# Optimization experiments

Measured on AMD Instinct MI355X. Metric: run time of the kernel, lower is better.

Reference implementation:

```python
import jax, jax.numpy as jnp
import numpy as np

NUM_TOKENS = 32000
N_EMBD = 2048
N_HEAD = 16
HEAD_SIZE = N_EMBD // N_HEAD
MAX_LEN = 2048
SEQ = 2048


def _make_pe(max_len, d_model):
    position = np.arange(max_len, dtype=np.float32)[:, None]
    emb_idx = np.arange(0, d_model, 2, dtype=np.float32)
    div_term = 1.0 / np.power(10000.0, emb_idx / d_model)
    pe = np.zeros((max_len, d_model), dtype=np.float32)
    pe[:, 0::2] = np.sin(position * div_term)
    pe[:, 1::2] = np.cos(position * div_term)
    return jnp.asarray(pe)


def setup_inputs() -> dict:
    key = jax.random.key(0)
    ks = jax.random.split(key, 8)
    s = 1.0 / np.sqrt(N_EMBD)
    return {
        "token_ids": jax.random.randint(ks[0], (SEQ,), 0, NUM_TOKENS, dtype=jnp.int32),
        "we": jax.random.normal(ks[1], (NUM_TOKENS, N_EMBD), dtype=jnp.float32),
        "pe": _make_pe(MAX_LEN, N_EMBD),
        "Wq": jax.random.normal(ks[2], (N_HEAD, N_EMBD, HEAD_SIZE), dtype=jnp.float32) * s,
        "Wk": jax.random.normal(ks[3], (N_HEAD, N_EMBD, HEAD_SIZE), dtype=jnp.float32) * s,
        "Wv": jax.random.normal(ks[4], (N_HEAD, N_EMBD, HEAD_SIZE), dtype=jnp.float32) * s,
        "proj_w": jax.random.normal(ks[5], (N_EMBD, N_EMBD), dtype=jnp.float32) * s,
        "proj_b": jnp.zeros((N_EMBD,), dtype=jnp.float32),
        "fc_w": jax.random.normal(ks[6], (N_EMBD, NUM_TOKENS), dtype=jnp.float32) * s,
        "fc_b": jnp.zeros((NUM_TOKENS,), dtype=jnp.float32),
    }


def reference(token_ids, we, pe, Wq, Wk, Wv, proj_w, proj_b, fc_w, fc_b):
    T = token_ids.shape[0]
    x = we[token_ids] + pe[:T]                      # [T, D]
    # per-head QKV, stacked over heads: [H, T, hs]
    q = jnp.einsum('td,hdk->htk', x, Wq)
    k = jnp.einsum('td,hdk->htk', x, Wk)
    v = jnp.einsum('td,hdk->htk', x, Wv)
    scale = 1.0 / jnp.sqrt(jnp.asarray(HEAD_SIZE, dtype=x.dtype))
    sims = jnp.einsum('htk,hsk->hts', q, k) * scale  # [H, T, T]
    causal = jnp.tril(jnp.ones((T, T), dtype=bool))  # mask==0 where NOT lower-tri
    sims = jnp.where(causal[None], sims, jnp.asarray(-1e9, dtype=x.dtype))
    attn = jax.nn.softmax(sims, axis=-1)
    heads = jnp.einsum('hts,hsk->htk', attn, v)      # [H, T, hs]
    cat = jnp.transpose(heads, (1, 0, 2)).reshape(T, N_HEAD * HEAD_SIZE)
    sa = cat @ proj_w + proj_b                       # dropout = identity (eval)
    resid = x + sa
    return resid @ fc_w + fc_b                       # [T, num_tokens]
```

## Files before the change

kernel.cpp:

```cpp
#include <hip/hip_runtime.h>

#define T_SEQ 2048
#define D_EMB 2048
#define NHEAD 16
#define HS    128
#define NVOC  32000

typedef __attribute__((ext_vector_type(8))) short bf16x8;
typedef __attribute__((ext_vector_type(4))) float f32x4;
typedef unsigned short bfu;

__device__ __forceinline__ f32x4 mfma16(bf16x8 a, bf16x8 b, f32x4 c) {
    return __builtin_amdgcn_mfma_f32_16x16x32_bf16(a, b, c, 0, 0, 0);
}

__device__ __forceinline__ bfu f2bu(float f) {
    unsigned int u = __float_as_uint(f);
    unsigned int r = (u + 0x7fffu + ((u >> 16) & 1u)) >> 16;
    return (bfu)r;
}
__device__ __forceinline__ float b2f(bfu r) {
    return __uint_as_float((unsigned int)r << 16);
}

__device__ __forceinline__ void async_copy16(void* lds, const void* g) {
    __builtin_amdgcn_global_load_lds(
        (const __attribute__((address_space(1))) unsigned int*)g,
        (__attribute__((address_space(3))) unsigned int*)lds, 16, 0, 0);
}

#define SB0 __builtin_amdgcn_sched_barrier(0)
#define BARRIER __builtin_amdgcn_s_barrier()
#define WAIT_VM8   asm volatile("s_waitcnt vmcnt(8)" ::: "memory")
#define WAIT_VM6   asm volatile("s_waitcnt vmcnt(6)" ::: "memory")
#define WAIT_VM4   asm volatile("s_waitcnt vmcnt(4)" ::: "memory")
#define WAIT_VM2   asm volatile("s_waitcnt vmcnt(2)" ::: "memory")
#define WAIT_VM0   asm volatile("s_waitcnt vmcnt(0)" ::: "memory")

__device__ __forceinline__ void job_t64(const float* __restrict__ in,
                                        bfu* __restrict__ out, int R, int C,
                                        float scale, int tx, int ty, char* lds) {
    float (*tile)[65] = (float(*)[65])lds;
    const int r0 = ty * 64, c0 = tx * 64;
    const int t = threadIdx.x;
#pragma unroll
    for (int it = 0; it < 4; ++it) {
        int fi = it * 256 + t;
        int row = fi >> 4, c4 = (fi & 15) * 4;
        float4 v = *(const float4*)(in + (size_t)(r0 + row) * C + c0 + c4);
        tile[row][c4]     = v.x; tile[row][c4 + 1] = v.y;
        tile[row][c4 + 2] = v.z; tile[row][c4 + 3] = v.w;
    }
    __syncthreads();
#pragma unroll
    for (int it = 0; it < 4; ++it) {
        int ci = it * 256 + t;
        int oc = ci >> 4, r4 = (ci & 15) * 4;
        ushort4 u;
        u.x = f2bu(tile[r4 + 0][oc] * scale);
        u.y = f2bu(tile[r4 + 1][oc] * scale);
        u.z = f2bu(tile[r4 + 2][oc] * scale);
        u.w = f2bu(tile[r4 + 3][oc] * scale);
        *(ushort4*)(out + (size_t)(c0 + oc) * R + r0 + r4) = u;
    }
}

__global__ __launch_bounds__(256)
void k_prep(const int* __restrict__ ids, const float* __restrict__ we,
            const float* __restrict__ pe, bfu* __restrict__ xb,
            const float* __restrict__ Wq, const float* __restrict__ Wk,
            const float* __restrict__ Wv, const float* __restrict__ projw,
            bfu* __restrict__ WqT, bfu* __restrict__ WkT, bfu* __restrict__ WvT,
            bfu* __restrict__ projT, float qscale) {
    __shared__ __align__(16) char lds[64 * 65 * 4];
    int b = blockIdx.x;
    if (b < 1024) {
        job_t64(projw, projT, D_EMB, D_EMB, 1.0f, b & 31, b >> 5, lds);
    } else if (b < 4096) {
        int bb = b - 1024;
        int which = bb >> 10;
        bb &= 1023;
        int z = bb >> 6, rem = bb & 63;
        size_t zo = (size_t)z * D_EMB * HS;
        const float* in = (which == 0) ? Wq : (which == 1) ? Wk : Wv;
        bfu* out = (which == 0) ? WqT : (which == 1) ? WkT : WvT;
        job_t64(in + zo, out + zo, D_EMB, HS, (which == 0) ? qscale : 1.0f,
                rem & 1, rem >> 1, lds);
    } else {
        int tt = b - 4096;
        const int row = ids[tt];
        const float4* wr = (const float4*)(we + (size_t)row * D_EMB);
        const float4* pr = (const float4*)(pe + (size_t)tt * D_EMB);
        bfu* xbr = xb + (size_t)tt * D_EMB;
        int i = threadIdx.x;
#pragma unroll
        for (int r = 0; r < 2; ++r, i += 256) {
            float4 a = wr[i], p = pr[i];
            ushort4 u;
            u.x = f2bu(a.x + p.x); u.y = f2bu(a.y + p.y);
            u.z = f2bu(a.z + p.z); u.w = f2bu(a.w + p.w);
            *(ushort4*)(xbr + i * 4) = u;
        }
    }
}

__global__ void k_transpose_bf(const bfu* __restrict__ in, bfu* __restrict__ out,
                               int stride, int Tout) {
    __shared__ bfu tile[64][72];
    const int r0 = blockIdx.x * 64;
    const int c0 = blockIdx.y * 64;
    const int t = threadIdx.x;
#pragma unroll
    for (int it = 0; it < 2; ++it) {
        int idx = it * 256 + t;
        int row = idx >> 3, c8 = (idx & 7) * 8;
        *(bf16x8*)&tile[row][c8] = *(const bf16x8*)(in + (size_t)(r0 + row) * stride + c0 + c8);
    }
    __syncthreads();
#pragma unroll
    for (int it = 0; it < 2; ++it) {
        int idx = it * 256 + t;
        int oc = idx >> 3, r8 = (idx & 7) * 8;
        bf16x8 v;
#pragma unroll
        for (int j = 0; j < 8; ++j) v[j] = (short)tile[r8 + j][oc];
        *(bf16x8*)(out + (size_t)(c0 + oc) * Tout + r0 + r8) = v;
    }
}

template <int EPI>
__global__ __launch_bounds__(256, 2)
void k_gemm_nt(const bfu* __restrict__ A, const bfu* __restrict__ Bt,
               bfu* __restrict__ Cv, const float* __restrict__ bias,
               const bfu* __restrict__ resb, int M, int N, int K) {
    __shared__ __align__(16) char smem[2 * 128 * 64 * 2];
    const int tid = threadIdx.x;
    const int w = tid >> 6, lane = tid & 63;
    const int wr = w >> 1, wc = w & 1;
    const int lr = lane & 15, lk = lane >> 4;
    const int sw = ((lk ^ (lr & 7)) << 4);
    const int mb = M >> 7;
    const int m0 = (blockIdx.x % mb) << 7;
    const int n0 = (blockIdx.x / mb) << 7;
    char* As = smem;
    char* Bs = smem + 16384;
    f32x4 acc[4][4];
#pragma unroll
    for (int i = 0; i < 4; ++i)
#pragma unroll
        for (int j = 0; j < 4; ++j) acc[i][j] = (f32x4){0.f, 0.f, 0.f, 0.f};

    const bfu* Ag = A + (size_t)m0 * K;
    const bfu* Bg = Bt + (size_t)n0 * K;

    for (int kk = 0; kk < K; kk += 64) {
        __syncthreads();
#pragma unroll
        for (int r = 0; r < 4; ++r) {
            int i = r * 256 + tid;
            int row = i >> 3, slot = (i & 7) ^ (row & 7);
            async_copy16(As + (r * 256 + w * 64) * 16,
                         Ag + (size_t)row * K + kk + slot * 8);
        }
#pragma unroll
        for (int r = 0; r < 4; ++r) {
            int i = r * 256 + tid;
            int row = i >> 3, slot = (i & 7) ^ (row & 7);
            async_copy16(Bs + (r * 256 + w * 64) * 16,
                         Bg + (size_t)row * K + kk + slot * 8);
        }
        __syncthreads();
#pragma unroll
        for (int kc = 0; kc < 2; ++kc) {
            const int so = kc ? (sw ^ 64) : sw;
            bf16x8 a[4], b[4];
#pragma unroll
            for (int mf = 0; mf < 4; ++mf)
                a[mf] = *(const bf16x8*)(As + (wr * 64 + mf * 16 + lr) * 128 + so);
#pragma unroll
            for (int nf = 0; nf < 4; ++nf)
                b[nf] = *(const bf16x8*)(Bs + (wc * 64 + nf * 16 + lr) * 128 + so);
#pragma unroll
            for (int mf = 0; mf < 4; ++mf)
#pragma unroll
                for (int nf = 0; nf < 4; ++nf)
                    acc[mf][nf] = mfma16(a[mf], b[nf], acc[mf][nf]);
        }
    }
#pragma unroll
    for (int nf = 0; nf < 4; ++nf) {
        int col = n0 + wc * 64 + nf * 16 + lr;
        float bv = (EPI >= 1) ? bias[col] : 0.0f;
#pragma unroll
        for (int mf = 0; mf < 4; ++mf) {
            int row0 = m0 + wr * 64 + mf * 16 + lk * 4;
            f32x4 v = acc[mf][nf];
#pragma unroll
            for (int j = 0; j < 4; ++j) {
                size_t idx = (size_t)(row0 + j) * N + col;
                float val = v[j] + bv;
                if (EPI == 1) val += b2f(resb[idx]);
                Cv[idx] = f2bu(val);
            }
        }
    }
}

__device__ __forceinline__ void stage_chunk(char* sm, const bfu* A_, const bfu* B_,
                                            int K, int tt, int kind, int w,
                                            int laneRow, int laneCol) {
    char* base = sm + (size_t)(tt & 1) * 65536 + ((kind >= 2) ? 32768 : 0);
    const bfu* G = (kind >= 2) ? B_ : A_;
#pragma unroll
    for (int r = 0; r < 2; ++r) {
        int p = w * 2 + r;
        int row0 = (kind < 2) ? ((kind & 1) * 64 + (p & 7) * 8 + (p >> 3) * 128)
                              : ((kind & 1) * 32 + (p & 3) * 8 + (p >> 2) * 64);
        const char* g = (const char*)G + ((size_t)(row0 + laneRow) * K + tt * 64) * 2 + laneCol;
        async_copy16(base + row0 * 128, g);
    }
}

template <int Q>
__device__ __forceinline__ void read_A(bf16x8 (&aA)[2][4][2], const char* bufA,
                                       int wm, int lr, int sw0) {
    const char* p = bufA + ((wm * 128 + Q * 64 + lr) * 128);
#pragma unroll
    for (int mf = 0; mf < 4; ++mf) {
        aA[Q][mf][0] = *(const bf16x8*)(p + mf * 2048 + sw0);
        aA[Q][mf][1] = *(const bf16x8*)(p + mf * 2048 + (sw0 ^ 64));
    }
}

template <int Q>
__device__ __forceinline__ void read_B(bf16x8 (&bB)[2][2], const char* bufB,
                                       int wn, int lr, int sw0) {
    const char* p = bufB + ((wn * 64 + Q * 32 + lr) * 128);
#pragma unroll
    for (int nf = 0; nf < 2; ++nf) {
        bB[nf][0] = *(const bf16x8*)(p + nf * 2048 + sw0);
        bB[nf][1] = *(const bf16x8*)(p + nf * 2048 + (sw0 ^ 64));
    }
}

template <int QM, int QN>
__device__ __forceinline__ void mfma_quad(f32x4 (&acc)[8][4], bf16x8 (&aA)[2][4][2],
                                          bf16x8 (&bB)[2][2]) {
    __builtin_amdgcn_s_setprio(1);
#pragma unroll
    for (int kc = 0; kc < 2; ++kc)
#pragma unroll
        for (int mf = 0; mf < 4; ++mf)
#pragma unroll
            for (int nf = 0; nf < 2; ++nf)
                acc[QM * 4 + mf][QN * 2 + nf] =
                    mfma16(aA[QM][mf][kc], bB[nf][kc], acc[QM * 4 + mf][QN * 2 + nf]);
    __builtin_amdgcn_s_setprio(0);
}

__device__ __forceinline__ void job_fcw512(const float* __restrict__ in,
                                           bfu* __restrict__ out, int tx, int ty,
                                           char* lds) {
    const int r0 = ty * 256, c0 = tx * 64;
    const int t = threadIdx.x;
#pragma unroll
    for (int it = 0; it < 8; ++it) {
        int fi = it * 512 + t;
        int row = fi >> 4, c4 = (fi & 15) * 4;
        float4 v = *(const float4*)(in + (size_t)(r0 + row) * NVOC + c0 + c4);
        ushort4 u;
        u.x = f2bu(v.x); u.y = f2bu(v.y); u.z = f2bu(v.z); u.w = f2bu(v.w);
        *(ushort4*)(lds + row * 128 + ((c4 * 2) ^ (((row >> 3) & 7) << 4))) = u;
    }
    __syncthreads();
#pragma unroll
    for (int it = 0; it < 4; ++it) {
        int idx = it * 512 + t;
        int oc = idx >> 5, r8 = (idx & 31) * 8;
        bf16x8 v;
#pragma unroll
        for (int j = 0; j < 8; ++j) {
            int row = r8 + j;
            v[j] = (short)*(const bfu*)(lds + row * 128 +
                                        ((oc * 2) ^ (((row >> 3) & 7) << 4)));
        }
        *(bf16x8*)(out + (size_t)(c0 + oc) * D_EMB + r0 + r8) = v;
    }
}

template <int EPI, bool FUSE_FCW>
__global__ __launch_bounds__(512, 2)
void k_gemm256(const bfu* __restrict__ A, const bfu* __restrict__ Bt,
               void* __restrict__ Cv, const float* __restrict__ bias,
               int M, int N, int K,
               const float* __restrict__ fcw, bfu* __restrict__ fcwT,
               int gemm_nwgs) {
    __shared__ __align__(16) char smem[2 * 65536];
    if (FUSE_FCW && (int)blockIdx.x >= gemm_nwgs) {
        int fb = blockIdx.x - gemm_nwgs;
        job_fcw512(fcw, fcwT, fb % 500, fb / 500, smem);
        return;
    }
    const int tid = threadIdx.x;
    const int w = tid >> 6, lane = tid & 63;
    const int wm = w >> 2, wn = w & 3;
    const int lr = lane & 15, lk = lane >> 4;
    const int sw0 = ((lk ^ (lr & 7)) << 4);
    const int laneRow = lane >> 3;
    const int laneCol = ((lane & 7) ^ (lane >> 3)) << 4;

    const int mb = M >> 8;
    const int nwgs = mb * (N >> 8);
    int bid = blockIdx.x;
    int swz = ((nwgs & 7) == 0) ? ((bid & 7) * (nwgs >> 3) + (bid >> 3)) : bid;
    const int m0 = (swz % mb) << 8;
    const int n0 = (swz / mb) << 8;

    const bfu* Ag = A + (size_t)m0 * K;
    const bfu* Bg = Bt + (size_t)n0 * K;

    f32x4 acc[8][4];
#pragma unroll
    for (int i = 0; i < 8; ++i)
#pragma unroll
        for (int j = 0; j < 4; ++j) acc[i][j] = (f32x4){0.f, 0.f, 0.f, 0.f};
    bf16x8 aA[2][4][2], bB[2][2];

    const int nkt = K >> 6;

    stage_chunk(smem, Ag, Bg, K, 0, 0, w, laneRow, laneCol);
    stage_chunk(smem, Ag, Bg, K, 0, 2, w, laneRow, laneCol);
    stage_chunk(smem, Ag, Bg, K, 0, 1, w, laneRow, laneCol);
    stage_chunk(smem, Ag, Bg, K, 0, 3, w, laneRow, laneCol);
    stage_chunk(smem, Ag, Bg, K, 1, 2, w, laneRow, laneCol);
    stage_chunk(smem, Ag, Bg, K, 1, 0, w, laneRow, laneCol);
    WAIT_VM8; SB0; BARRIER;

    for (int t = 0; t < nkt - 2; ++t) {
        const char* bufA = smem + (size_t)(t & 1) * 65536;
        const char* bufB = bufA + 32768;
        read_A<0>(aA, bufA, wm, lr, sw0);
        read_B<0>(bB, bufB, wn, lr, sw0);
        stage_chunk(smem, Ag, Bg, K, t + 1, 1, w, laneRow, laneCol);
        mfma_quad<0, 0>(acc, aA, bB);
        WAIT_VM8; BARRIER;

        read_A<1>(aA, bufA, wm, lr, sw0);
        stage_chunk(smem, Ag, Bg, K, t + 1, 3, w, laneRow, laneCol);
        mfma_quad<1, 0>(acc, aA, bB);
        WAIT_VM8; BARRIER;

        read_B<1>(bB, bufB, wn, lr, sw0);
        stage_chunk(smem, Ag, Bg, K, t + 2, 2, w, laneRow, laneCol);
        mfma_quad<0, 1>(acc, aA, bB);
        WAIT_VM8; BARRIER;

        stage_chunk(smem, Ag, Bg, K, t + 2, 0, w, laneRow, laneCol);
        mfma_quad<1, 1>(acc, aA, bB);
        WAIT_VM8; BARRIER;
    }

    {
        const int t = nkt - 2;
        const char* bufA = smem + (size_t)(t & 1) * 65536;
        const char* bufB = bufA + 32768;
        read_A<0>(aA, bufA, wm, lr, sw0);
        read_B<0>(bB, bufB, wn, lr, sw0);
        stage_chunk(smem, Ag, Bg, K, t + 1, 1, w, laneRow, laneCol);
        mfma_quad<0, 0>(acc, aA, bB);
        WAIT_VM8; BARRIER;

        read_A<1>(aA, bufA, wm, lr, sw0);
        stage_chunk(smem, Ag, Bg, K, t + 1, 3, w, laneRow, laneCol);
        mfma_quad<1, 0>(acc, aA, bB);
        WAIT_VM8; BARRIER;

        read_B<1>(bB, bufB, wn, lr, sw0);
        mfma_quad<0, 1>(acc, aA, bB);
        WAIT_VM6; BARRIER;

        mfma_quad<1, 1>(acc, aA, bB);
        WAIT_VM4; BARRIER;
    }
    {
        const int t = nkt - 1;
        const char* bufA = smem + (size_t)(t & 1) * 65536;
        const char* bufB = bufA + 32768;
        read_A<0>(aA, bufA, wm, lr, sw0);
        read_B<0>(bB, bufB, wn, lr, sw0);
        mfma_quad<0, 0>(acc, aA, bB);
        WAIT_VM2; BARRIER;

        read_A<1>(aA, bufA, wm, lr, sw0);
        mfma_quad<1, 0>(acc, aA, bB);
        WAIT_VM0; BARRIER;

        read_B<1>(bB, bufB, wn, lr, sw0);
        mfma_quad<0, 1>(acc, aA, bB);
        mfma_quad<1, 1>(acc, aA, bB);
    }

#pragma unroll
    for (int nfg = 0; nfg < 4; ++nfg) {
        int col = n0 + wn * 64 + nfg * 16 + lr;
        float bv = (EPI == 2) ? bias[col] : 0.0f;
#pragma unroll
        for (int mfg = 0; mfg < 8; ++mfg) {
            int row0 = m0 + wm * 128 + mfg * 16 + lk * 4;
            f32x4 v = acc[mfg][nfg];
#pragma unroll
            for (int j = 0; j < 4; ++j) {
                size_t idx = (size_t)(row0 + j) * N + col;
                if (EPI == 2) ((float*)Cv)[idx] = v[j] + bv;
                else          ((bfu*)Cv)[idx] = f2bu(v[j]);
            }
        }
    }
}

__global__ __launch_bounds__(256, 2)
void k_attn(const bfu* __restrict__ q, const bfu* __restrict__ k,
            const bfu* __restrict__ vT, bfu* __restrict__ o, int qks) {
    __shared__ __align__(16) char kvlds[2][32768];
    __shared__ __align__(16) bfu plds[4][16][72];
    const int w = threadIdx.x >> 6, lane = threadIdx.x & 63;
    const int lr = lane & 15, lk = lane >> 4;
    const int h = blockIdx.y;
    const int bxr = (gridDim.x - 1) - blockIdx.x;
    const int qrow = bxr * 64 + w * 16;
    const int sw = ((lk ^ (lr & 7)) << 4);

    const int krow = lane >> 4, kslot = lane & 15;
    const int vrow = lane >> 3, vslot = lane & 7;

    bf16x8 aq[4];
#pragma unroll
    for (int kc = 0; kc < 4; ++kc)
        aq[kc] = *(const bf16x8*)(q + (size_t)(qrow + lr) * qks + h * HS + kc * 32 + lk * 8);

    f32x4 O[8];
#pragma unroll
    for (int hf = 0; hf < 8; ++hf) O[hf] = (f32x4){0.f, 0.f, 0.f, 0.f};
    float m_[4], l_[4];
#pragma unroll
    for (int j = 0; j < 4; ++j) { m_[j] = -__builtin_inff(); l_[j] = 0.f; }

    const int nst = bxr + 1;

#define STAGE_KV(st)                                                            \
    {                                                                           \
        char* bK = kvlds[(st) & 1];                                             \
        char* bV = bK + 16384;                                                  \
        const int s0_ = (st) * 64;                                              \
        _Pragma("unroll")                                                       \
        for (int j = 0; j < 4; ++j) {                                           \
            int ir = w * 4 + j;                                                 \
            int krw = ir * 4 + krow;                                            \
            int kss = (kslot & 8) | ((kslot & 7) ^ (krw & 7));                  \
            async_copy16(bK + ir * 1024,                                        \
                         k + (size_t)(s0_ + krw) * qks + h * HS + kss * 8);     \
            int vrw = ir * 8 + vrow;                                            \
            int vss = vslot ^ (vrw & 7);                                        \
            async_copy16(bV + ir * 1024,                                        \
                         vT + (size_t)(h * HS + vrw) * T_SEQ + s0_ + vss * 8);  \
        }                                                                       \
    }

    STAGE_KV(0);
    WAIT_VM0; BARRIER;

    for (int st = 0; st < nst; ++st) {
        const char* bK = kvlds[st & 1];
        const char* bV = bK + 16384;
        const int s0 = st * 64;
        if (st + 1 < nst) STAGE_KV(st + 1);

        f32x4 S[4];
#pragma unroll
        for (int nf = 0; nf < 4; ++nf) S[nf] = (f32x4){0.f, 0.f, 0.f, 0.f};
#pragma unroll
        for (int nf = 0; nf < 4; ++nf) {
            const char* kp = bK + (nf * 16 + lr) * 256;
#pragma unroll
            for (int kc = 0; kc < 4; ++kc) {
                bf16x8 bk = *(const bf16x8*)(kp + ((kc & 2) << 6) + (sw ^ ((kc & 1) << 6)));
                S[nf] = mfma16(aq[kc], bk, S[nf]);
            }
        }
        if (s0 + 63 > qrow) {
#pragma unroll
            for (int nf = 0; nf < 4; ++nf) {
                int scol = s0 + nf * 16 + lr;
#pragma unroll
                for (int j = 0; j < 4; ++j)
                    if (scol > qrow + lk * 4 + j) S[nf][j] = -1e30f;
            }
        }
        float tm[4];
#pragma unroll
        for (int j = 0; j < 4; ++j)
            tm[j] = fmaxf(fmaxf(S[0][j], S[1][j]), fmaxf(S[2][j], S[3][j]));
#pragma unroll
        for (int d = 1; d < 16; d <<= 1)
#pragma unroll
            for (int j = 0; j < 4; ++j) tm[j] = fmaxf(tm[j], __shfl_xor(tm[j], d));
        float mn[4], ts[4];
#pragma unroll
        for (int j = 0; j < 4; ++j) mn[j] = fmaxf(m_[j], tm[j]);
#pragma unroll
        for (int nf = 0; nf < 4; ++nf)
#pragma unroll
            for (int j = 0; j < 4; ++j) S[nf][j] = __expf(S[nf][j] - mn[j]);
#pragma unroll
        for (int j = 0; j < 4; ++j) ts[j] = S[0][j] + S[1][j] + S[2][j] + S[3][j];
#pragma unroll
        for (int d = 1; d < 16; d <<= 1)
#pragma unroll
            for (int j = 0; j < 4; ++j) ts[j] += __shfl_xor(ts[j], d);
#pragma unroll
        for (int nf = 0; nf < 4; ++nf)
#pragma unroll
            for (int j = 0; j < 4; ++j)
                plds[w][lk * 4 + j][nf * 16 + lr] = f2bu(S[nf][j]);
#pragma unroll
        for (int j = 0; j < 4; ++j) {
            float f = __expf(m_[j] - mn[j]);
            l_[j] = l_[j] * f + ts[j];
            m_[j] = mn[j];
#pragma unroll
            for (int hf = 0; hf < 8; ++hf) O[hf][j] *= f;
        }
        bf16x8 pa[2];
#pragma unroll
        for (int kc2 = 0; kc2 < 2; ++kc2)
            pa[kc2] = *(const bf16x8*)(&plds[w][lr][kc2 * 32 + lk * 8]);
#pragma unroll
        for (int hf = 0; hf < 8; ++hf) {
            const char* vp = bV + (hf * 16 + lr) * 128;
#pragma unroll
            for (int kc2 = 0; kc2 < 2; ++kc2) {
                bf16x8 bv = *(const bf16x8*)(vp + (sw ^ (kc2 << 6)));
                O[hf] = mfma16(pa[kc2], bv, O[hf]);
            }
        }
        WAIT_VM0; BARRIER;
    }
#undef STAGE_KV

#pragma unroll
    for (int j = 0; j < 4; ++j) {
        float inv = 1.0f / l_[j];
        size_t rbase = (size_t)(qrow + lk * 4 + j) * D_EMB + h * HS;
#pragma unroll
        for (int hf = 0; hf < 8; ++hf)
            o[rbase + hf * 16 + lr] = f2bu(O[hf][j] * inv);
    }
}

extern "C" void kernel_launch(void* const* d_in, const int* in_sizes, int n_in,
                              void* d_out, int out_size, void* d_ws, size_t ws_size,
                              hipStream_t stream) {
    const int*   ids   = (const int*)d_in[0];
    const float* we    = (const float*)d_in[1];
    const float* pe    = (const float*)d_in[2];
    const float* Wq    = (const float*)d_in[3];
    const float* Wk    = (const float*)d_in[4];
    const float* Wv    = (const float*)d_in[5];
    const float* projw = (const float*)d_in[6];
    const float* projb = (const float*)d_in[7];
    const float* fcw   = (const float*)d_in[8];
    const float* fcb   = (const float*)d_in[9];
    float* out = (float*)d_out;
    (void)in_sizes; (void)n_in; (void)out_size; (void)ws_size;

    char* ws = (char*)d_ws;
    size_t off = 0;
    bfu*   fcwT  = (bfu*)(ws + off);  off += (size_t)NVOC * D_EMB * 2;
    bfu*   xb    = (bfu*)(ws + off);  off += (size_t)T_SEQ * D_EMB * 2;
    bfu*   qkvb  = (bfu*)(ws + off);  off += (size_t)T_SEQ * 3 * D_EMB * 2;
    bfu*   vTb   = (bfu*)(ws + off);  off += (size_t)D_EMB * T_SEQ * 2;
    bfu*   WqT   = (bfu*)(ws + off);  off += (size_t)D_EMB * D_EMB * 2;
    bfu*   WkT   = (bfu*)(ws + off);  off += (size_t)D_EMB * D_EMB * 2;
    bfu*   WvT   = (bfu*)(ws + off);  off += (size_t)D_EMB * D_EMB * 2;
    bfu*   projT = (bfu*)(ws + off);  off += (size_t)D_EMB * D_EMB * 2;
    bfu*   attnb = WqT;
    bfu*   resb  = WvT;

    const float qscale = 0.08838834764831845f;

    k_prep<<<6144, 256, 0, stream>>>(ids, we, pe, xb, Wq, Wk, Wv, projw,
                                     WqT, WkT, WvT, projT, qscale);

    k_gemm256<0, true><<<192 + 4000, 512, 0, stream>>>(
        xb, WqT, qkvb, nullptr, T_SEQ, 3 * D_EMB, D_EMB, fcw, fcwT, 192);

    k_transpose_bf<<<dim3(T_SEQ / 64, D_EMB / 64), 256, 0, stream>>>(
        qkvb + 2 * D_EMB, vTb, 3 * D_EMB, T_SEQ);

    k_attn<<<dim3(T_SEQ / 64, NHEAD), 256, 0, stream>>>(qkvb, qkvb + D_EMB, vTb, attnb, 3 * D_EMB);

    k_gemm_nt<1><<<(T_SEQ / 128) * (D_EMB / 128), 256, 0, stream>>>(
        attnb, projT, resb, projb, xb, T_SEQ, D_EMB, D_EMB);

    k_gemm256<2, false><<<(T_SEQ / 256) * (NVOC / 256), 512, 0, stream>>>(
        resb, fcwT, out, fcb, T_SEQ, NVOC, D_EMB, nullptr, nullptr, 0);
}
```

Measured before the change: 568.0 us.

## Prefetch next-tile LDS fragments into double-buffered registers during MFMA quads

Gives the B fragments a second register buffer (one per half-tile) so each quad reads the next A/B half from LDS before issuing the current MFMAs. The first-quad fragments of the next k-tile are loaded early, during the last quad of the current tile, and the wait counts and barriers are reshuffled to match, with one barrier dropping its vmcnt wait. The aim is to hide LDS read latency behind MFMA work. It costs more VGPRs and adds a risk of subtle read/write hazards on the shared buffers if the barrier placement is wrong.

```diff
diff --git a/kernel.cpp b/kernel.cpp
--- a/kernel.cpp
+++ b/kernel.cpp
@@ -233,19 +233,19 @@
 }
 
 template <int Q>
-__device__ __forceinline__ void read_B(bf16x8 (&bB)[2][2], const char* bufB,
+__device__ __forceinline__ void read_B(bf16x8 (&bB)[2][2][2], const char* bufB,
                                        int wn, int lr, int sw0) {
     const char* p = bufB + ((wn * 64 + Q * 32 + lr) * 128);
 #pragma unroll
     for (int nf = 0; nf < 2; ++nf) {
-        bB[nf][0] = *(const bf16x8*)(p + nf * 2048 + sw0);
-        bB[nf][1] = *(const bf16x8*)(p + nf * 2048 + (sw0 ^ 64));
+        bB[Q][nf][0] = *(const bf16x8*)(p + nf * 2048 + sw0);
+        bB[Q][nf][1] = *(const bf16x8*)(p + nf * 2048 + (sw0 ^ 64));
     }
 }
 
 template <int QM, int QN>
 __device__ __forceinline__ void mfma_quad(f32x4 (&acc)[8][4], bf16x8 (&aA)[2][4][2],
-                                          bf16x8 (&bB)[2][2]) {
+                                          bf16x8 (&bB)[2][2][2]) {
     __builtin_amdgcn_s_setprio(1);
 #pragma unroll
     for (int kc = 0; kc < 2; ++kc)
@@ -254,7 +254,7 @@
 #pragma unroll
             for (int nf = 0; nf < 2; ++nf)
                 acc[QM * 4 + mf][QN * 2 + nf] =
-                    mfma16(aA[QM][mf][kc], bB[nf][kc], acc[QM * 4 + mf][QN * 2 + nf]);
+                    mfma16(aA[QM][mf][kc], bB[QN][nf][kc], acc[QM * 4 + mf][QN * 2 + nf]);
     __builtin_amdgcn_s_setprio(0);
 }
 
@@ -324,7 +324,7 @@
     for (int i = 0; i < 8; ++i)
 #pragma unroll
         for (int j = 0; j < 4; ++j) acc[i][j] = (f32x4){0.f, 0.f, 0.f, 0.f};
-    bf16x8 aA[2][4][2], bB[2][2];
+    bf16x8 aA[2][4][2], bB[2][2][2];
 
     const int nkt = K >> 6;
 
@@ -334,68 +334,67 @@
     stage_chunk(smem, Ag, Bg, K, 0, 3, w, laneRow, laneCol);
     stage_chunk(smem, Ag, Bg, K, 1, 2, w, laneRow, laneCol);
     stage_chunk(smem, Ag, Bg, K, 1, 0, w, laneRow, laneCol);
-    WAIT_VM8; SB0; BARRIER;
+    WAIT_VM6; SB0; BARRIER;
+    read_A<0>(aA, smem, wm, lr, sw0);
+    read_B<0>(bB, smem + 32768, wn, lr, sw0);
 
     for (int t = 0; t < nkt - 2; ++t) {
         const char* bufA = smem + (size_t)(t & 1) * 65536;
         const char* bufB = bufA + 32768;
-        read_A<0>(aA, bufA, wm, lr, sw0);
-        read_B<0>(bB, bufB, wn, lr, sw0);
+        const char* bufAn = smem + (size_t)((t + 1) & 1) * 65536;
+        const char* bufBn = bufAn + 32768;
+        read_A<1>(aA, bufA, wm, lr, sw0);
         stage_chunk(smem, Ag, Bg, K, t + 1, 1, w, laneRow, laneCol);
         mfma_quad<0, 0>(acc, aA, bB);
-        WAIT_VM8; BARRIER;
-
-        read_A<1>(aA, bufA, wm, lr, sw0);
+        WAIT_VM6; BARRIER;
+        read_B<1>(bB, bufB, wn, lr, sw0);
         stage_chunk(smem, Ag, Bg, K, t + 1, 3, w, laneRow, laneCol);
         mfma_quad<1, 0>(acc, aA, bB);
-        WAIT_VM8; BARRIER;
-
-        read_B<1>(bB, bufB, wn, lr, sw0);
+        BARRIER;
         stage_chunk(smem, Ag, Bg, K, t + 2, 2, w, laneRow, laneCol);
         mfma_quad<0, 1>(acc, aA, bB);
-        WAIT_VM8; BARRIER;
-
+        WAIT_VM6; BARRIER;
+        read_A<0>(aA, bufAn, wm, lr, sw0);
+        read_B<0>(bB, bufBn, wn, lr, sw0);
         stage_chunk(smem, Ag, Bg, K, t + 2, 0, w, laneRow, laneCol);
         mfma_quad<1, 1>(acc, aA, bB);
-        WAIT_VM8; BARRIER;
+        WAIT_VM6; BARRIER;
     }
 
     {
         const int t = nkt - 2;
         const char* bufA = smem + (size_t)(t & 1) * 65536;
         const char* bufB = bufA + 32768;
-        read_A<0>(aA, bufA, wm, lr, sw0);
-        read_B<0>(bB, bufB, wn, lr, sw0);
+        const char* bufAn = smem + (size_t)((t + 1) & 1) * 65536;
+        const char* bufBn = bufAn + 32768;
+        read_A<1>(aA, bufA, wm, lr, sw0);
         stage_chunk(smem, Ag, Bg, K, t + 1, 1, w, laneRow, laneCol);
         mfma_quad<0, 0>(acc, aA, bB);
-        WAIT_VM8; BARRIER;
-
-        read_A<1>(aA, bufA, wm, lr, sw0);
+        WAIT_VM6; BARRIER;
+
+        read_B<1>(bB, bufB, wn, lr, sw0);
         stage_chunk(smem, Ag, Bg, K, t + 1, 3, w, laneRow, laneCol);
         mfma_quad<1, 0>(acc, aA, bB);
-        WAIT_VM8; BARRIER;
-
-        read_B<1>(bB, bufB, wn, lr, sw0);
+        BARRIER;
+
         mfma_quad<0, 1>(acc, aA, bB);
-        WAIT_VM6; BARRIER;
-
+        WAIT_VM4; BARRIER;
+
+        read_A<0>(aA, bufAn, wm, lr, sw0);
+        read_B<0>(bB, bufBn, wn, lr, sw0);
         mfma_quad<1, 1>(acc, aA, bB);
-        WAIT_VM4; BARRIER;
+        WAIT_VM2; BARRIER;
     }
     {
         const int t = nkt - 1;
         const char* bufA = smem + (size_t)(t & 1) * 65536;
         const char* bufB = bufA + 32768;
-        read_A<0>(aA, bufA, wm, lr, sw0);
-        read_B<0>(bB, bufB, wn, lr, sw0);
+        read_A<1>(aA, bufA, wm, lr, sw0);
         mfma_quad<0, 0>(acc, aA, bB);
-        WAIT_VM2; BARRIER;
-
-        read_A<1>(aA, bufA, wm, lr, sw0);
+        WAIT_VM0; BARRIER;
+
+        read_B<1>(bB, bufB, wn, lr, sw0);
         mfma_quad<1, 0>(acc, aA, bB);
-        WAIT_VM0; BARRIER;
-
-        read_B<1>(bB, bufB, wn, lr, sw0);
         mfma_quad<0, 1>(acc, aA, bB);
         mfma_quad<1, 1>(acc, aA, bB);
     }
```

New measurement: 606.2 us. 6.7% more time.

## Move fc_w bf16 transpose from QKV GEMM launch into attention kernel grid

Applied to the files above, without the earlier changes.

The fp32-to-bf16 transpose of fc_w was previously appended as extra workgroups to the QKV GEMM launch. It now runs as extra workgroups in the attention kernel grid, using a 256-thread variant of the transpose job. Attention blocks come first in block order, so the memory-bound conversion blocks can fill CUs left idle by the causal-attention tail. The risk is that conversion traffic contends with attention for bandwidth, and the larger LDS footprint of the attention kernel limits how many conversion blocks fit per CU.

```diff
diff --git a/kernel.cpp b/kernel.cpp
--- a/kernel.cpp
+++ b/kernel.cpp
@@ -62,6 +62,36 @@
         u.z = f2bu(tile[r4 + 2][oc] * scale);
         u.w = f2bu(tile[r4 + 3][oc] * scale);
         *(ushort4*)(out + (size_t)(c0 + oc) * R + r0 + r4) = u;
+    }
+}
+
+__device__ __forceinline__ void job_fcw256(const float* __restrict__ in,
+                                           bfu* __restrict__ out, int tx, int ty,
+                                           char* lds) {
+    const int r0 = ty * 256, c0 = tx * 64;
+    const int t = threadIdx.x;
+#pragma unroll
+    for (int it = 0; it < 16; ++it) {
+        int fi = it * 256 + t;
+        int row = fi >> 4, c4 = (fi & 15) * 4;
+        float4 v = *(const float4*)(in + (size_t)(r0 + row) * NVOC + c0 + c4);
+        ushort4 u;
+        u.x = f2bu(v.x); u.y = f2bu(v.y); u.z = f2bu(v.z); u.w = f2bu(v.w);
+        *(ushort4*)(lds + row * 128 + ((c4 * 2) ^ (((row >> 3) & 7) << 4))) = u;
+    }
+    __syncthreads();
+#pragma unroll
+    for (int it = 0; it < 8; ++it) {
+        int idx = it * 256 + t;
+        int oc = idx >> 5, r8 = (idx & 31) * 8;
+        bf16x8 v;
+#pragma unroll
+        for (int j = 0; j < 8; ++j) {
+            int row = r8 + j;
+            v[j] = (short)*(const bfu*)(lds + row * 128 +
+                                        ((oc * 2) ^ (((row >> 3) & 7) << 4)));
+        }
+        *(bf16x8*)(out + (size_t)(c0 + oc) * D_EMB + r0 + r8) = v;
     }
 }
 
@@ -258,49 +288,12 @@
     __builtin_amdgcn_s_setprio(0);
 }
 
-__device__ __forceinline__ void job_fcw512(const float* __restrict__ in,
-                                           bfu* __restrict__ out, int tx, int ty,
-                                           char* lds) {
-    const int r0 = ty * 256, c0 = tx * 64;
-    const int t = threadIdx.x;
-#pragma unroll
-    for (int it = 0; it < 8; ++it) {
-        int fi = it * 512 + t;
-        int row = fi >> 4, c4 = (fi & 15) * 4;
-        float4 v = *(const float4*)(in + (size_t)(r0 + row) * NVOC + c0 + c4);
-        ushort4 u;
-        u.x = f2bu(v.x); u.y = f2bu(v.y); u.z = f2bu(v.z); u.w = f2bu(v.w);
-        *(ushort4*)(lds + row * 128 + ((c4 * 2) ^ (((row >> 3) & 7) << 4))) = u;
-    }
-    __syncthreads();
-#pragma unroll
-    for (int it = 0; it < 4; ++it) {
-        int idx = it * 512 + t;
-        int oc = idx >> 5, r8 = (idx & 31) * 8;
-        bf16x8 v;
-#pragma unroll
-        for (int j = 0; j < 8; ++j) {
-            int row = r8 + j;
-            v[j] = (short)*(const bfu*)(lds + row * 128 +
-                                        ((oc * 2) ^ (((row >> 3) & 7) << 4)));
-        }
-        *(bf16x8*)(out + (size_t)(c0 + oc) * D_EMB + r0 + r8) = v;
-    }
-}
-
-template <int EPI, bool FUSE_FCW>
+template <int EPI>
 __global__ __launch_bounds__(512, 2)
 void k_gemm256(const bfu* __restrict__ A, const bfu* __restrict__ Bt,
                void* __restrict__ Cv, const float* __restrict__ bias,
-               int M, int N, int K,
-               const float* __restrict__ fcw, bfu* __restrict__ fcwT,
-               int gemm_nwgs) {
+               int M, int N, int K) {
     __shared__ __align__(16) char smem[2 * 65536];
-    if (FUSE_FCW && (int)blockIdx.x >= gemm_nwgs) {
-        int fb = blockIdx.x - gemm_nwgs;
-        job_fcw512(fcw, fcwT, fb % 500, fb / 500, smem);
-        return;
-    }
     const int tid = threadIdx.x;
     const int w = tid >> 6, lane = tid & 63;
     const int wm = w >> 2, wn = w & 3;
@@ -420,13 +413,19 @@
 
 __global__ __launch_bounds__(256, 2)
 void k_attn(const bfu* __restrict__ q, const bfu* __restrict__ k,
-            const bfu* __restrict__ vT, bfu* __restrict__ o, int qks) {
+            const bfu* __restrict__ vT, bfu* __restrict__ o, int qks,
+            const float* __restrict__ fcw, bfu* __restrict__ fcwT) {
     __shared__ __align__(16) char kvlds[2][32768];
     __shared__ __align__(16) bfu plds[4][16][72];
+    if ((int)blockIdx.x >= 32) {
+        int fb = ((int)blockIdx.x - 32) + 250 * (int)blockIdx.y;
+        job_fcw256(fcw, fcwT, fb % 500, fb / 500, (char*)kvlds);
+        return;
+    }
     const int w = threadIdx.x >> 6, lane = threadIdx.x & 63;
     const int lr = lane & 15, lk = lane >> 4;
     const int h = blockIdx.y;
-    const int bxr = (gridDim.x - 1) - blockIdx.x;
+    const int bxr = 31 - (int)blockIdx.x;
     const int qrow = bxr * 64 + w * 16;
     const int sw = ((lk ^ (lr & 7)) << 4);
 
@@ -591,17 +590,18 @@
     k_prep<<<6144, 256, 0, stream>>>(ids, we, pe, xb, Wq, Wk, Wv, projw,
                                      WqT, WkT, WvT, projT, qscale);
 
-    k_gemm256<0, true><<<192 + 4000, 512, 0, stream>>>(
-        xb, WqT, qkvb, nullptr, T_SEQ, 3 * D_EMB, D_EMB, fcw, fcwT, 192);
+    k_gemm256<0><<<(T_SEQ / 256) * (3 * D_EMB / 256), 512, 0, stream>>>(
+        xb, WqT, qkvb, nullptr, T_SEQ, 3 * D_EMB, D_EMB);
 
     k_transpose_bf<<<dim3(T_SEQ / 64, D_EMB / 64), 256, 0, stream>>>(
         qkvb + 2 * D_EMB, vTb, 3 * D_EMB, T_SEQ);
 
-    k_attn<<<dim3(T_SEQ / 64, NHEAD), 256, 0, stream>>>(qkvb, qkvb + D_EMB, vTb, attnb, 3 * D_EMB);
+    k_attn<<<dim3(32 + 250, NHEAD), 256, 0, stream>>>(
+        qkvb, qkvb + D_EMB, vTb, attnb, 3 * D_EMB, fcw, fcwT);
 
     k_gemm_nt<1><<<(T_SEQ / 128) * (D_EMB / 128), 256, 0, stream>>>(
         attnb, projT, resb, projb, xb, T_SEQ, D_EMB, D_EMB);
 
-    k_gemm256<2, false><<<(T_SEQ / 256) * (NVOC / 256), 512, 0, stream>>>(
-        resb, fcwT, out, fcb, T_SEQ, NVOC, D_EMB, nullptr, nullptr, 0);
-}
+    k_gemm256<2><<<(T_SEQ / 256) * (NVOC / 256), 512, 0, stream>>>(
+        resb, fcwT, out, fcb, T_SEQ, NVOC, D_EMB);
+}
```

Measured after the change: 560.1 us. About the same (-1.4%).
